# Performance work log

Hardware: AMD Instinct MI355X
Metric: run time of the kernel (lower is better)

## Reference

```python
import jax, jax.numpy as jnp
import numpy as np

D_K = 64

def setup_inputs() -> dict:
    key = jax.random.key(0)
    k1, k2, k3, k4 = jax.random.split(key, 4)
    B, H, S, D = 2, 16, 2048, D_K
    Q = jax.random.normal(k1, (B, H, S, D), dtype=jnp.float32)
    K = jax.random.normal(k2, (B, H, S, D), dtype=jnp.float32)
    V = jax.random.normal(k3, (B, H, S, D), dtype=jnp.float32)
    attn_mask = jax.random.randint(k4, (B, H, S, S), 0, 2).astype(jnp.bool_)
    return {"Q": Q, "K": K, "V": V, "attn_mask": attn_mask}

def reference(Q, K, V, attn_mask):
    # scores: [B, H, S, S]
    scale = 1.0 / np.sqrt(D_K).astype(np.float32)
    scores = jnp.einsum('bhqd,bhkd->bhqk', Q, K) * scale
    scores = jnp.where(attn_mask, jnp.float32(-1e9), scores)
    attn = jax.nn.softmax(scores, axis=-1)
    context = jnp.einsum('bhqk,bhkd->bhqd', attn, V)
    return (context, attn)
```

## Files before the change

kernel.cpp:

```cpp
#include <hip/hip_runtime.h>
#include <hip/hip_bf16.h>


#define S_LEN 2048
#define D_DIM 64
#define NKT 32
#define QB 64

typedef __attribute__((ext_vector_type(8))) short bf16x8;
typedef __attribute__((ext_vector_type(4))) float f32x4;
typedef __attribute__((ext_vector_type(4))) unsigned short us4;

__device__ __forceinline__ unsigned short f2bf(float f) {
    return __builtin_bit_cast(unsigned short, __float2bfloat16(f));
}
__device__ __forceinline__ float bf2f(unsigned short b) {
    return __builtin_bit_cast(float, (unsigned)b << 16);
}

typedef const __attribute__((address_space(1))) void cg_void;
typedef __attribute__((address_space(3))) void lds_void;
__device__ __forceinline__ void gload16(const void* g, void* l) {
    __builtin_amdgcn_global_load_lds((cg_void*)g, (lds_void*)l, 16, 0, 0);
}

__global__ __launch_bounds__(256)
void sdpa_prep(const float* __restrict__ K, const float* __restrict__ V,
               unsigned short* __restrict__ Kimg, unsigned short* __restrict__ Vimg)
{
    const int blk = blockIdx.x;
    const int bh = blk >> 5, kt = blk & 31;
    const float* Kt = K + ((size_t)bh * S_LEN + kt * 64) * D_DIM;
    const float* Vt = V + ((size_t)bh * S_LEN + kt * 64) * D_DIM;
    unsigned char* Kd = (unsigned char*)(Kimg + (size_t)blk * 4096);
    unsigned char* Vd = (unsigned char*)(Vimg + (size_t)blk * 4096);
    const int tid = threadIdx.x;

    {
        const int srow = tid >> 4, c4 = tid & 15;
        #pragma unroll
        for (int i = 0; i < 4; ++i) {
            int row = srow + i * 16;
            float4 v = *(const float4*)(Kt + (size_t)row * D_DIM + c4 * 4);
            us4 b = { f2bf(v.x), f2bf(v.y), f2bf(v.z), f2bf(v.w) };
            *(us4*)(Kd + row * 128 + (((c4 >> 1) ^ (row & 7)) << 4) + (c4 & 1) * 8) = b;
        }
    }
    {
        const int d = tid & 63, kg = tid >> 6;
        #pragma unroll
        for (int kk = 0; kk < 4; ++kk) {
            int k4 = kg * 4 + kk;
            int k0 = k4 * 4;
            float v0 = Vt[(size_t)(k0 + 0) * D_DIM + d];
            float v1 = Vt[(size_t)(k0 + 1) * D_DIM + d];
            float v2 = Vt[(size_t)(k0 + 2) * D_DIM + d];
            float v3 = Vt[(size_t)(k0 + 3) * D_DIM + d];
            us4 b = { f2bf(v0), f2bf(v1), f2bf(v2), f2bf(v3) };
            *(us4*)(Vd + d * 128 + (((k4 >> 1) ^ (d & 7)) << 4) + (k4 & 1) * 8) = b;
        }
    }
}

__global__ __launch_bounds__(256, 4)
void sdpa_main(const float* __restrict__ Q,
               const int* __restrict__ M,
               const unsigned short* __restrict__ Kimg,
               const unsigned short* __restrict__ Vimg,
               float* __restrict__ ctx_out,
               float* __restrict__ attn_out)
{
    __shared__ __align__(16) unsigned char smem[40960];
    unsigned short* const sK0 = (unsigned short*)(smem);
    unsigned short* const sK1 = (unsigned short*)(smem + 8192);
    unsigned short* const sV0 = (unsigned short*)(smem + 16384);
    unsigned short* const sV1 = (unsigned short*)(smem + 24576);
    unsigned short* const sPB = (unsigned short*)(smem + 32768);
    unsigned short* const sQl = (unsigned short*)(smem + 32768);

    const int tid  = threadIdx.x;
    const int lane = tid & 63;
    const int w    = tid >> 6;
    const int lq   = lane & 15;
    const int h    = lane >> 4;
    const int l7   = lq & 7;

    int b   = blockIdx.x;
    int swz = (b & 7) * 128 + (b >> 3);
    int bh  = swz >> 5, qt = swz & 31;
    const int q0 = qt * QB;

    const float* Qh = Q + ((size_t)bh * S_LEN + q0) * D_DIM;
    const int*   Mh = M + (size_t)bh * S_LEN * S_LEN;
    const unsigned short* Kh = Kimg + (size_t)bh * NKT * 4096;
    const unsigned short* Vh = Vimg + (size_t)bh * NKT * 4096;
    float* Ah = attn_out + (size_t)bh * S_LEN * S_LEN;
    float* Ch = ctx_out  + (size_t)bh * S_LEN * D_DIM;

    const int kf0 = ((h)     ^ l7) << 3;
    const int kf1 = ((4 + h) ^ l7) << 3;

    const int* Mb = Mh + (size_t)(q0 + w * 16 + h * 4) * S_LEN + lq;

    unsigned bits[4][4];
    #pragma unroll
    for (int jt = 0; jt < 4; ++jt)
        #pragma unroll
        for (int r = 0; r < 4; ++r)
            bits[jt][r] = 0u;

    #pragma unroll
    for (int tt = 0; tt < 2; ++tt)
        #pragma unroll
        for (int i = 0; i < 2; ++i)
            gload16((const unsigned char*)(Kh + (size_t)tt * 4096) + w * 2048 + i * 1024 + lane * 16,
                    smem + tt * 8192 + w * 2048 + i * 1024);
    __builtin_amdgcn_sched_barrier(0);

    #pragma unroll
    for (int tt = 0; tt < 2; ++tt)
        #pragma unroll
        for (int jt = 0; jt < 4; ++jt)
            #pragma unroll
            for (int r = 0; r < 4; ++r) {
                int m = __builtin_nontemporal_load(&Mb[(size_t)r * S_LEN + tt * 64 + jt * 16]);
                bits[jt][r] |= (m ? 1u : 0u) << tt;
            }

    const float SC = 0.18033688011112042f;
    {
        const int srow = tid >> 4, c4 = tid & 15;
        #pragma unroll
        for (int i = 0; i < 4; ++i) {
            int row = srow + i * 16;
            float4 v = *(const float4*)(Qh + (size_t)row * D_DIM + c4 * 4);
            us4 bq = { f2bf(v.x * SC), f2bf(v.y * SC), f2bf(v.z * SC), f2bf(v.w * SC) };
            *(us4*)((unsigned char*)sQl + row * 128 + (((c4 >> 1) ^ (row & 7)) << 4) + (c4 & 1) * 8) = bq;
        }
    }
    __syncthreads();

    bf16x8 aq0 = *(const bf16x8*)(&sQl[(w * 16 + lq) * 64 + kf0]);
    bf16x8 aq1 = *(const bf16x8*)(&sQl[(w * 16 + lq) * 64 + kf1]);

    float lsum[4];
    #pragma unroll
    for (int r = 0; r < 4; ++r) lsum[r] = 0.f;

    for (int s = 0; s < 16; ++s) {
        const int kt0 = 2 * s;
        unsigned char* curp = smem + (s & 1) * 16384;
        unsigned char* nxtp = smem + ((s & 1) ^ 1) * 16384;
        const bool more = (s + 1 < 16);

        if (more) {
            #pragma unroll
            for (int tt = 0; tt < 2; ++tt)
                #pragma unroll
                for (int i = 0; i < 2; ++i)
                    gload16((const unsigned char*)(Kh + (size_t)(kt0 + 2 + tt) * 4096) + w * 2048 + i * 1024 + lane * 16,
                            nxtp + tt * 8192 + w * 2048 + i * 1024);
        }
        __builtin_amdgcn_sched_barrier(0);

        int mn[2][4][4];
        if (more) {
            #pragma unroll
            for (int tt = 0; tt < 2; ++tt)
                #pragma unroll
                for (int jt = 0; jt < 4; ++jt)
                    #pragma unroll
                    for (int r = 0; r < 4; ++r)
                        mn[tt][jt][r] = __builtin_nontemporal_load(
                            &Mb[(size_t)r * S_LEN + (kt0 + 2 + tt) * 64 + jt * 16]);
        }

        #pragma unroll
        for (int tt = 0; tt < 2; ++tt) {
            const unsigned short* kbuf = (const unsigned short*)(curp + tt * 8192);
            f32x4 acc[4];
            __builtin_amdgcn_s_setprio(1);
            #pragma unroll
            for (int jt = 0; jt < 4; ++jt) {
                acc[jt] = (f32x4){0.f, 0.f, 0.f, 0.f};
                const unsigned short* kb = kbuf + (jt * 16 + lq) * 64;
                bf16x8 b0 = *(const bf16x8*)(kb + kf0);
                bf16x8 b1 = *(const bf16x8*)(kb + kf1);
                acc[jt] = __builtin_amdgcn_mfma_f32_16x16x32_bf16(aq0, b0, acc[jt], 0, 0, 0);
                acc[jt] = __builtin_amdgcn_mfma_f32_16x16x32_bf16(aq1, b1, acc[jt], 0, 0, 0);
            }
            __builtin_amdgcn_s_setprio(0);
            #pragma unroll
            for (int r = 0; r < 4; ++r) {
                float e[4];
                #pragma unroll
                for (int jt = 0; jt < 4; ++jt) {
                    unsigned msk = (bits[jt][r] >> (kt0 + tt)) & 1u;
                    float ev = exp2f(acc[jt][r]);
                    e[jt] = msk ? 0.f : ev;
                }
                lsum[r] += (e[0] + e[1]) + (e[2] + e[3]);
            }
        }

        if (more) {
            #pragma unroll
            for (int tt = 0; tt < 2; ++tt)
                #pragma unroll
                for (int jt = 0; jt < 4; ++jt)
                    #pragma unroll
                    for (int r = 0; r < 4; ++r)
                        bits[jt][r] |= (mn[tt][jt][r] ? 1u : 0u) << (kt0 + 2 + tt);
        }
        __syncthreads();
    }

    float myIL[4];
    #pragma unroll
    for (int r = 0; r < 4; ++r) {
        float li = lsum[r];
        #pragma unroll
        for (int off = 1; off < 16; off <<= 1)
            li += __shfl_xor(li, off);
        myIL[r] = (li > 0.f) ? (1.f / li) : 0.f;
    }

    #pragma unroll
    for (int i = 0; i < 2; ++i) {
        gload16((const unsigned char*)Kh + w * 2048 + i * 1024 + lane * 16,
                (unsigned char*)sK0 + w * 2048 + i * 1024);
        gload16((const unsigned char*)Vh + w * 2048 + i * 1024 + lane * 16,
                (unsigned char*)sV0 + w * 2048 + i * 1024);
    }
    __syncthreads();

    f32x4 ctxa[4];
    #pragma unroll
    for (int dt = 0; dt < 4; ++dt) ctxa[dt] = (f32x4){0.f, 0.f, 0.f, 0.f};

    unsigned short* const sPw = sPB + w * 1024;
    float* const Abase = Ah + (size_t)(q0 + w * 16) * S_LEN;

    auto step2 = [&](unsigned short* curK, unsigned short* curV,
                     unsigned short* nxtK, unsigned short* nxtV, int kt) {
        const int ktn = (kt + 1 < NKT) ? kt + 1 : kt;
        #pragma unroll
        for (int i = 0; i < 2; ++i) {
            gload16((const unsigned char*)(Kh + (size_t)ktn * 4096) + w * 2048 + i * 1024 + lane * 16,
                    (unsigned char*)nxtK + w * 2048 + i * 1024);
            gload16((const unsigned char*)(Vh + (size_t)ktn * 4096) + w * 2048 + i * 1024 + lane * 16,
                    (unsigned char*)nxtV + w * 2048 + i * 1024);
        }
        __builtin_amdgcn_sched_barrier(0);

        f32x4 acc[4];
        __builtin_amdgcn_s_setprio(1);
        #pragma unroll
        for (int jt = 0; jt < 4; ++jt) {
            acc[jt] = (f32x4){0.f, 0.f, 0.f, 0.f};
            const unsigned short* kb = curK + (jt * 16 + lq) * 64;
            bf16x8 b0 = *(const bf16x8*)(kb + kf0);
            bf16x8 b1 = *(const bf16x8*)(kb + kf1);
            acc[jt] = __builtin_amdgcn_mfma_f32_16x16x32_bf16(aq0, b0, acc[jt], 0, 0, 0);
            acc[jt] = __builtin_amdgcn_mfma_f32_16x16x32_bf16(aq1, b1, acc[jt], 0, 0, 0);
        }
        __builtin_amdgcn_s_setprio(0);

        #pragma unroll
        for (int jt = 0; jt < 4; ++jt)
            #pragma unroll
            for (int r = 0; r < 4; ++r) {
                bool msk = (bits[jt][r] >> kt) & 1u;
                float p = exp2f(acc[jt][r]) * myIL[r];
                p = msk ? 0.f : p;
                int row = h * 4 + r;
                sPw[row * 64 + ((((jt << 1) | (lq >> 3)) ^ (row & 7)) << 3) + l7] = f2bf(p);
            }
        asm volatile("s_waitcnt lgkmcnt(0)" ::: "memory");
        __builtin_amdgcn_sched_barrier(0);

        float* Aw = Abase + kt * 64;
        #pragma unroll
        for (int it = 0; it < 4; ++it) {
            int row = it * 4 + h;
            us4 pb = *(const us4*)(&sPw[row * 64 + (((lq >> 1) ^ (row & 7)) << 3) + (lq & 1) * 4]);
            f32x4 pf = { bf2f(pb.x), bf2f(pb.y), bf2f(pb.z), bf2f(pb.w) };
            __builtin_nontemporal_store(pf, (f32x4*)(Aw + (size_t)row * S_LEN + lq * 4));
        }

        bf16x8 pa0 = *(const bf16x8*)(&sPw[lq * 64 + ((h ^ l7) << 3)]);
        bf16x8 pa1 = *(const bf16x8*)(&sPw[lq * 64 + (((4 + h) ^ l7) << 3)]);
        __builtin_amdgcn_s_setprio(1);
        #pragma unroll
        for (int dt = 0; dt < 4; ++dt) {
            const unsigned short* vb = curV + (dt * 16 + lq) * 64;
            bf16x8 b0 = *(const bf16x8*)(vb + kf0);
            bf16x8 b1 = *(const bf16x8*)(vb + kf1);
            ctxa[dt] = __builtin_amdgcn_mfma_f32_16x16x32_bf16(pa0, b0, ctxa[dt], 0, 0, 0);
            ctxa[dt] = __builtin_amdgcn_mfma_f32_16x16x32_bf16(pa1, b1, ctxa[dt], 0, 0, 0);
        }
        __builtin_amdgcn_s_setprio(0);
        __syncthreads();
    };

    for (int kt = 0; kt < NKT; kt += 2) {
        step2(sK0, sV0, sK1, sV1, kt);
        step2(sK1, sV1, sK0, sV0, kt + 1);
    }

    float* Crow = Ch + (size_t)(q0 + w * 16 + h * 4) * D_DIM;
    #pragma unroll
    for (int dt = 0; dt < 4; ++dt)
        #pragma unroll
        for (int r = 0; r < 4; ++r)
            __builtin_nontemporal_store(ctxa[dt][r],
                Crow + (size_t)r * D_DIM + dt * 16 + lq);
}

extern "C" void kernel_launch(void* const* d_in, const int* in_sizes, int n_in,
                              void* d_out, int out_size, void* d_ws, size_t ws_size,
                              hipStream_t stream)
{
    const float* Q = (const float*)d_in[0];
    const float* K = (const float*)d_in[1];
    const float* V = (const float*)d_in[2];
    const int*   M = (const int*)d_in[3];

    float* ctx  = (float*)d_out;
    float* attn = ctx + (size_t)2 * 16 * S_LEN * D_DIM;

    const size_t imgElems = (size_t)32 * NKT * 4096;
    if (ws_size < 2 * imgElems * sizeof(unsigned short)) return;
    unsigned short* Kimg = (unsigned short*)d_ws;
    unsigned short* Vimg = Kimg + imgElems;

    sdpa_prep<<<dim3(1024), 256, 0, stream>>>(K, V, Kimg, Vimg);
    sdpa_main<<<dim3(1024), 256, 0, stream>>>(Q, M, Kimg, Vimg, ctx, attn);
}
```

Before: 277.6 us.

## Pack attention mask into bitmask in separate kernel, stage in ctx output buffer

```diff
diff --git a/kernel.cpp b/kernel.cpp
--- a/kernel.cpp
+++ b/kernel.cpp
@@ -62,9 +62,31 @@
     }
 }
 
+__global__ __launch_bounds__(256)
+void sdpa_mask(const int* __restrict__ M, unsigned* __restrict__ Bimg)
+{
+    const int blk = blockIdx.x;
+    const int bh = blk >> 7, qg = blk & 127;
+    const int tid = threadIdx.x;
+    const int wv = tid >> 6, lane = tid & 63;
+    const int q = qg * 16 + wv * 4;
+    const int* Mq = M + ((size_t)bh * S_LEN + q) * S_LEN;
+    unsigned* Bq = Bimg + ((size_t)bh * S_LEN + q) * 64;
+
+    #pragma unroll
+    for (int r = 0; r < 4; ++r) {
+        unsigned word = 0;
+        #pragma unroll 8
+        for (int kt = 0; kt < 32; ++kt) {
+            int m = __builtin_nontemporal_load(&Mq[(size_t)r * S_LEN + kt * 64 + lane]);
+            word |= (m ? 1u : 0u) << kt;
+        }
+        Bq[r * 64 + lane] = word;
+    }
+}
+
 __global__ __launch_bounds__(256, 4)
 void sdpa_main(const float* __restrict__ Q,
-               const int* __restrict__ M,
                const unsigned short* __restrict__ Kimg,
                const unsigned short* __restrict__ Vimg,
                float* __restrict__ ctx_out,
@@ -91,7 +113,6 @@
     const int q0 = qt * QB;
 
     const float* Qh = Q + ((size_t)bh * S_LEN + q0) * D_DIM;
-    const int*   Mh = M + (size_t)bh * S_LEN * S_LEN;
     const unsigned short* Kh = Kimg + (size_t)bh * NKT * 4096;
     const unsigned short* Vh = Vimg + (size_t)bh * NKT * 4096;
     float* Ah = attn_out + (size_t)bh * S_LEN * S_LEN;
@@ -100,14 +121,14 @@
     const int kf0 = ((h)     ^ l7) << 3;
     const int kf1 = ((4 + h) ^ l7) << 3;
 
-    const int* Mb = Mh + (size_t)(q0 + w * 16 + h * 4) * S_LEN + lq;
-
+    const unsigned* Bb = (const unsigned*)ctx_out
+                       + ((size_t)bh * S_LEN + q0 + w * 16 + h * 4) * 64;
     unsigned bits[4][4];
     #pragma unroll
-    for (int jt = 0; jt < 4; ++jt)
-        #pragma unroll
-        for (int r = 0; r < 4; ++r)
-            bits[jt][r] = 0u;
+    for (int r = 0; r < 4; ++r)
+        #pragma unroll
+        for (int jt = 0; jt < 4; ++jt)
+            bits[jt][r] = Bb[r * 64 + jt * 16 + lq];
 
     #pragma unroll
     for (int tt = 0; tt < 2; ++tt)
@@ -116,16 +137,6 @@
             gload16((const unsigned char*)(Kh + (size_t)tt * 4096) + w * 2048 + i * 1024 + lane * 16,
                     smem + tt * 8192 + w * 2048 + i * 1024);
     __builtin_amdgcn_sched_barrier(0);
-
-    #pragma unroll
-    for (int tt = 0; tt < 2; ++tt)
-        #pragma unroll
-        for (int jt = 0; jt < 4; ++jt)
-            #pragma unroll
-            for (int r = 0; r < 4; ++r) {
-                int m = __builtin_nontemporal_load(&Mb[(size_t)r * S_LEN + tt * 64 + jt * 16]);
-                bits[jt][r] |= (m ? 1u : 0u) << tt;
-            }
 
     const float SC = 0.18033688011112042f;
     {
@@ -162,18 +173,6 @@
                             nxtp + tt * 8192 + w * 2048 + i * 1024);
         }
         __builtin_amdgcn_sched_barrier(0);
-
-        int mn[2][4][4];
-        if (more) {
-            #pragma unroll
-            for (int tt = 0; tt < 2; ++tt)
-                #pragma unroll
-                for (int jt = 0; jt < 4; ++jt)
-                    #pragma unroll
-                    for (int r = 0; r < 4; ++r)
-                        mn[tt][jt][r] = __builtin_nontemporal_load(
-                            &Mb[(size_t)r * S_LEN + (kt0 + 2 + tt) * 64 + jt * 16]);
-        }
 
         #pragma unroll
         for (int tt = 0; tt < 2; ++tt) {
@@ -202,16 +201,6 @@
                 lsum[r] += (e[0] + e[1]) + (e[2] + e[3]);
             }
         }
-
-        if (more) {
-            #pragma unroll
-            for (int tt = 0; tt < 2; ++tt)
-                #pragma unroll
-                for (int jt = 0; jt < 4; ++jt)
-                    #pragma unroll
-                    for (int r = 0; r < 4; ++r)
-                        bits[jt][r] |= (mn[tt][jt][r] ? 1u : 0u) << (kt0 + 2 + tt);
-        }
         __syncthreads();
     }
 
@@ -335,5 +324,6 @@
     unsigned short* Vimg = Kimg + imgElems;
 
     sdpa_prep<<<dim3(1024), 256, 0, stream>>>(K, V, Kimg, Vimg);
-    sdpa_main<<<dim3(1024), 256, 0, stream>>>(Q, M, Kimg, Vimg, ctx, attn);
-}
+    sdpa_mask<<<dim3(4096), 256, 0, stream>>>(M, (unsigned*)ctx);
+    sdpa_main<<<dim3(1024), 256, 0, stream>>>(Q, Kimg, Vimg, ctx, attn);
+}
```

Measured after the change: 247.7 us. 10.8% less time.
